# Optimization experiments

Hardware: AMD Instinct MI355X
Metric: run time of the kernel (lower is better)

The kernel has to match this reference:

```python
import jax, jax.numpy as jnp
import numpy as np

SEG = 8  # conv1d groups


def _grouped_mix(y, W2, b2, seg):
    # y: [b, C_in, L]; W2: [C_out, C_in//seg]; grouped 1x1 conv1d
    b_, cin, L = y.shape
    cout = W2.shape[0]
    yg = y.reshape(b_, seg, cin // seg, L)
    Wg = W2.reshape(seg, cout // seg, cin // seg)
    z = jnp.einsum('bgcl,goc->bgol', yg, Wg).reshape(b_, cout, L)
    return z + b2[None, :, None]


def _mix_h(x, W1, b1, W2, b2):
    # x: [b,h,w,d]
    b_, H, Wd, D = x.shape
    y = jnp.einsum('bhwd,ed->bhwe', x, W1) + b1            # 1x1 conv2d -> [b,h,w,e]
    y = jnp.transpose(y, (0, 3, 1, 2)).reshape(b_, -1, Wd)  # 'b d h w -> b (d h) w'
    z = _grouped_mix(y, W2, b2, SEG)                        # [b, h*h, w]
    attn = jax.nn.softmax(
        z.reshape(b_, H, H, Wd).transpose(0, 3, 1, 2), axis=-1)  # [b,w,h1,h2]
    xr = jnp.transpose(x, (0, 2, 1, 3))                     # [b,w,h,d]
    out = jnp.einsum('bwij,bwjd->bwid', attn, xr)
    return jnp.transpose(out, (0, 2, 1, 3))                 # [b,h,w,d]


def _mix_w(x, W1, b1, W2, b2):
    # x: [b,h,w,d]
    b_, H, Wd, D = x.shape
    y = jnp.einsum('bhwd,ed->bhwe', x, W1) + b1             # [b,h,w,e]
    y = jnp.transpose(y, (0, 3, 2, 1)).reshape(b_, -1, H)   # 'b d w h -> b (d w) h'
    z = _grouped_mix(y, W2, b2, SEG)                        # [b, w*w, h]
    attn = jax.nn.softmax(
        z.reshape(b_, Wd, Wd, H).transpose(0, 3, 1, 2), axis=-1)  # [b,h,w1,w2]
    return jnp.einsum('bhij,bhjd->bhid', attn, x)           # [b,h,w,d]


def setup_inputs() -> dict:
    key = jax.random.key(0)
    ks = jax.random.split(key, 16)
    B, H, W, D, E = 64, 32, 32, 384, 2
    s = 0.05
    return {
        'x':   jax.random.normal(ks[0], (B, H, W, D), jnp.float32),
        'Wc':  jax.random.normal(ks[1], (D, D), jnp.float32) * s,
        'bc':  jnp.zeros((D,), jnp.float32),
        'Wo':  jax.random.normal(ks[2], (D, D), jnp.float32) * s,
        'bo':  jnp.zeros((D,), jnp.float32),
        'W1h': jax.random.normal(ks[3], (E, D), jnp.float32) * s,
        'b1h': jnp.zeros((E,), jnp.float32),
        'W2h': jax.random.normal(ks[4], (H * H, E * H // SEG), jnp.float32) * s,
        'b2h': jnp.zeros((H * H,), jnp.float32),
        'W1w': jax.random.normal(ks[5], (E, D), jnp.float32) * s,
        'b1w': jnp.zeros((E,), jnp.float32),
        'W2w': jax.random.normal(ks[6], (W * W, E * W // SEG), jnp.float32) * s,
        'b2w': jnp.zeros((W * W,), jnp.float32),
    }


def reference(x, Wc, bc, Wo, bo, W1h, b1h, W2h, b2h, W1w, b1w, W2w, b2w):
    Y_c = jnp.einsum('bhwd,od->bhwo', x, Wc) + bc
    Y_h = _mix_h(x, W1h, b1h, W2h, b2h)
    Y_w = _mix_w(x, W1w, b1w, W2w, b2w)
    Y = Y_h + Y_w + Y_c
    return jnp.einsum('bhwd,od->bhwo', Y, Wo) + bo
```

## Files before the change

### kernel.cpp

```cpp
#include <hip/hip_runtime.h>
#include <hip/hip_bf16.h>
#include <cstdint>
#include <cstddef>

typedef __bf16 bf16;
typedef __attribute__((ext_vector_type(8))) __bf16 bf16x8;
typedef __attribute__((ext_vector_type(4))) float floatx4;

#define NPIX 65536

__device__ inline void async_copy16(void* lds, const void* g) {
    __builtin_amdgcn_global_load_lds(
        (const __attribute__((address_space(1))) void*)g,
        (__attribute__((address_space(3))) void*)lds, 16, 0, 0);
}

__global__ void k_prep_w(const float* __restrict__ Wc, const float* __restrict__ bc,
                         const float* __restrict__ Wo, const float* __restrict__ bo,
                         bf16* __restrict__ Wfull, float* __restrict__ bco) {
    int blk = blockIdx.x;
    int t = threadIdx.x;
    if (blk < 384) {
        int o = blk;
        float acc = 0.f;
        for (int d = 0; d < 384; ++d)
            acc += Wo[o * 384 + d] * Wc[d * 384 + t];
        Wfull[(size_t)o * 768 + t]       = (bf16)Wo[o * 384 + t];
        Wfull[(size_t)o * 768 + 384 + t] = (bf16)acc;
    } else {
        int o = t;
        float acc = bo[o];
        for (int d = 0; d < 384; ++d)
            acc += Wo[o * 384 + d] * bc[d];
        bco[o] = acc;
    }
}

__global__ void k_proj(const float* __restrict__ xf, bf16* __restrict__ xb,
                       const float* __restrict__ W1h, const float* __restrict__ b1h,
                       const float* __restrict__ W1w, const float* __restrict__ b1w,
                       float* __restrict__ yh, float* __restrict__ yw) {
    int t  = threadIdx.x;
    int lg = t & 7;
    int pg = t >> 3;
    int p  = blockIdx.x * 32 + pg;
    int b = p >> 10, h = (p >> 5) & 31, w = p & 31;
    const float4* xp4 = (const float4*)(xf + (size_t)p * 384);
    float a0 = 0.f, a1 = 0.f, a2 = 0.f, a3 = 0.f;
#pragma unroll
    for (int j = 0; j < 6; ++j) {
        int c = j * 8 + lg;
        float4 xa = xp4[c * 2], xcv = xp4[c * 2 + 1];
        bf16x8 v;
        v[0] = (bf16)xa.x; v[1] = (bf16)xa.y; v[2] = (bf16)xa.z; v[3] = (bf16)xa.w;
        v[4] = (bf16)xcv.x; v[5] = (bf16)xcv.y; v[6] = (bf16)xcv.z; v[7] = (bf16)xcv.w;
        *(bf16x8*)(xb + (size_t)p * 384 + c * 8) = v;
        const float4* h0 = (const float4*)(W1h + c * 8);
        const float4* h1 = (const float4*)(W1h + 384 + c * 8);
        const float4* w0 = (const float4*)(W1w + c * 8);
        const float4* w1 = (const float4*)(W1w + 384 + c * 8);
        float4 h0a = h0[0], h0b = h0[1], h1a = h1[0], h1b = h1[1];
        float4 w0a = w0[0], w0b = w0[1], w1a = w1[0], w1b = w1[1];
        a0 += xa.x*h0a.x + xa.y*h0a.y + xa.z*h0a.z + xa.w*h0a.w
            + xcv.x*h0b.x + xcv.y*h0b.y + xcv.z*h0b.z + xcv.w*h0b.w;
        a1 += xa.x*h1a.x + xa.y*h1a.y + xa.z*h1a.z + xa.w*h1a.w
            + xcv.x*h1b.x + xcv.y*h1b.y + xcv.z*h1b.z + xcv.w*h1b.w;
        a2 += xa.x*w0a.x + xa.y*w0a.y + xa.z*w0a.z + xa.w*w0a.w
            + xcv.x*w0b.x + xcv.y*w0b.y + xcv.z*w0b.z + xcv.w*w0b.w;
        a3 += xa.x*w1a.x + xa.y*w1a.y + xa.z*w1a.z + xa.w*w1a.w
            + xcv.x*w1b.x + xcv.y*w1b.y + xcv.z*w1b.z + xcv.w*w1b.w;
    }
#pragma unroll
    for (int m = 1; m < 8; m <<= 1) {
        a0 += __shfl_xor(a0, m, 64);
        a1 += __shfl_xor(a1, m, 64);
        a2 += __shfl_xor(a2, m, 64);
        a3 += __shfl_xor(a3, m, 64);
    }
    if (lg == 0) {
        yh[((b * 2 + 0) * 32 + h) * 32 + w] = a0 + b1h[0];
        yh[((b * 2 + 1) * 32 + h) * 32 + w] = a1 + b1h[1];
        yw[((b * 2 + 0) * 32 + w) * 32 + h] = a2 + b1w[0];
        yw[((b * 2 + 1) * 32 + w) * 32 + h] = a3 + b1w[1];
    }
}

__global__ void k_attn(const float* __restrict__ yproj,
                       const float* __restrict__ W2, const float* __restrict__ b2,
                       bf16* __restrict__ attn) {
    int blk = blockIdx.x;
    int bi = blk >> 5, r1 = blk & 31;
    int g = r1 >> 2;
    int cb = g * 8;
    int e = cb >> 5, rb = cb & 31;
    int lane = threadIdx.x;
    int l = lane & 31, half = lane >> 5;
    float yv[8];
    const float* ybase = yproj + (((bi * 2 + e) * 32 + rb) * 32 + l);
#pragma unroll
    for (int c = 0; c < 8; ++c) yv[c] = ybase[c * 32];
    float z[16];
#pragma unroll
    for (int jj = 0; jj < 16; ++jj) {
        int r2 = half * 16 + jj;
        int row = r1 * 32 + r2;
        const float4* wp = (const float4*)(W2 + (size_t)row * 8);
        float4 wa = wp[0], wb = wp[1];
        z[jj] = b2[row]
              + yv[0]*wa.x + yv[1]*wa.y + yv[2]*wa.z + yv[3]*wa.w
              + yv[4]*wb.x + yv[5]*wb.y + yv[6]*wb.z + yv[7]*wb.w;
    }
    float m = -1e30f;
#pragma unroll
    for (int jj = 0; jj < 16; ++jj) m = fmaxf(m, z[jj]);
    m = fmaxf(m, __shfl_xor(m, 32, 64));
    float s = 0.f;
#pragma unroll
    for (int jj = 0; jj < 16; ++jj) { z[jj] = __expf(z[jj] - m); s += z[jj]; }
    s += __shfl_xor(s, 32, 64);
    float inv = 1.f / s;
    bf16x8 o0, o1;
#pragma unroll
    for (int jj = 0; jj < 8; ++jj) o0[jj] = (bf16)(z[jj] * inv);
#pragma unroll
    for (int jj = 0; jj < 8; ++jj) o1[jj] = (bf16)(z[8 + jj] * inv);
    bf16x8* dst = (bf16x8*)(attn + ((((size_t)bi * 32 + l) * 32 + r1) * 32 + half * 16));
    dst[0] = o0;
    dst[1] = o1;
}

__global__ __launch_bounds__(256) void k_mix(const bf16* __restrict__ x,
                                             const bf16* __restrict__ attn_h,
                                             const bf16* __restrict__ attn_w,
                                             bf16* __restrict__ T) {
    __shared__ bf16 Xs[1024 * 16];
    __shared__ bf16 Ts[1024 * 16];
    int n = blockIdx.x;
    int a = n >> 5, r = n & 31;
    int q = a * 8 + (r & 7);
    int bi = q / 6, cq = q % 6;
    int c = cq * 4 + (r >> 3);
    int dbase = c * 16;
    int tid = threadIdx.x;
    int wv = tid >> 6, lane = tid & 63;
    int n16 = lane & 15, quad = lane >> 4;

    const char* gbase = (const char*)(x + (size_t)bi * 1024 * 384 + dbase);
#pragma unroll
    for (int it = 0; it < 8; ++it) {
        int p0 = wv * 256 + it * 32;
        const char* g = gbase + (size_t)(p0 + (lane >> 1)) * 768 + (lane & 1) * 16;
        char* l = (char*)Xs + p0 * 32 + lane * 16;
        async_copy16(l, g);
    }
    __syncthreads();

#pragma unroll
    for (int wl = 0; wl < 8; ++wl) {
        int w = wv * 8 + wl;
        const bf16* ab = attn_h + ((size_t)(bi * 32 + w) * 32) * 32;
        bf16x8 af0 = *(const bf16x8*)(ab + n16 * 32 + quad * 8);
        bf16x8 af1 = *(const bf16x8*)(ab + (16 + n16) * 32 + quad * 8);
        bf16x8 bfrag;
#pragma unroll
        for (int i = 0; i < 8; ++i) {
            int j = quad * 8 + i;
            bfrag[i] = Xs[(j * 32 + w) * 16 + n16];
        }
        floatx4 c0 = {0.f, 0.f, 0.f, 0.f}, c1 = {0.f, 0.f, 0.f, 0.f};
        c0 = __builtin_amdgcn_mfma_f32_16x16x32_bf16(af0, bfrag, c0, 0, 0, 0);
        c1 = __builtin_amdgcn_mfma_f32_16x16x32_bf16(af1, bfrag, c1, 0, 0, 0);
#pragma unroll
        for (int rr = 0; rr < 4; ++rr) {
            int h0 = quad * 4 + rr;
            Ts[(h0 * 32 + w) * 16 + n16]        = (bf16)c0[rr];
            Ts[((16 + h0) * 32 + w) * 16 + n16] = (bf16)c1[rr];
        }
    }
    __syncthreads();

#pragma unroll
    for (int hl = 0; hl < 8; ++hl) {
        int h = wv * 8 + hl;
        const bf16* ab = attn_w + ((size_t)(bi * 32 + h) * 32) * 32;
        bf16x8 af0 = *(const bf16x8*)(ab + n16 * 32 + quad * 8);
        bf16x8 af1 = *(const bf16x8*)(ab + (16 + n16) * 32 + quad * 8);
        bf16x8 bfrag;
#pragma unroll
        for (int i = 0; i < 8; ++i) {
            int j = quad * 8 + i;
            bfrag[i] = Xs[(h * 32 + j) * 16 + n16];
        }
        floatx4 c0 = {0.f, 0.f, 0.f, 0.f}, c1 = {0.f, 0.f, 0.f, 0.f};
        c0 = __builtin_amdgcn_mfma_f32_16x16x32_bf16(af0, bfrag, c0, 0, 0, 0);
        c1 = __builtin_amdgcn_mfma_f32_16x16x32_bf16(af1, bfrag, c1, 0, 0, 0);
        bf16* Tr = T + ((size_t)(bi * 32 + h) * 32) * 384 + dbase;
#pragma unroll
        for (int rr = 0; rr < 4; ++rr) {
            int w0 = quad * 4 + rr;
            Tr[(size_t)w0 * 384 + n16] =
                (bf16)(c0[rr] + (float)Ts[(h * 32 + w0) * 16 + n16]);
            Tr[(size_t)(16 + w0) * 384 + n16] =
                (bf16)(c1[rr] + (float)Ts[(h * 32 + 16 + w0) * 16 + n16]);
        }
    }
}

#define LDP 72
__global__ __launch_bounds__(256) void k_gemm(const bf16* __restrict__ T, const bf16* __restrict__ x,
                                              const bf16* __restrict__ Wfull, const float* __restrict__ bco,
                                              float* __restrict__ out) {
    __shared__ bf16 As[128 * LDP];
    __shared__ bf16 Bs[128 * LDP];
    int bx = blockIdx.x;
    int gid = (bx & 7) * 192 + (bx >> 3);
    int nt = gid % 3, pt = gid / 3;
    int obase = nt * 128;
    int pbase = pt * 128;
    int tid = threadIdx.x;
    int wv = tid >> 6, lane = tid & 63;
    int wm = wv & 1, wn = wv >> 1;
    int n16 = lane & 15, quad = lane >> 4;
    int lrow = tid >> 3;
    int lchunk = tid & 7;
    floatx4 zero = {0.f, 0.f, 0.f, 0.f};
    floatx4 acc[4][4];
#pragma unroll
    for (int i = 0; i < 4; ++i)
#pragma unroll
        for (int j = 0; j < 4; ++j) acc[i][j] = zero;

    for (int kt = 0; kt < 12; ++kt) {
        const bf16* Asrc = (kt < 6) ? (T + (size_t)pbase * 384 + kt * 64)
                                    : (x + (size_t)pbase * 384 + (kt - 6) * 64);
        const bf16* Bsrc = Wfull + (size_t)obase * 768 + kt * 64;
        bf16x8 av[4], bv[4];
#pragma unroll
        for (int s = 0; s < 4; ++s)
            av[s] = *(const bf16x8*)(Asrc + (size_t)(s * 32 + lrow) * 384 + lchunk * 8);
#pragma unroll
        for (int s = 0; s < 4; ++s)
            bv[s] = *(const bf16x8*)(Bsrc + (size_t)(s * 32 + lrow) * 768 + lchunk * 8);
        __syncthreads();
#pragma unroll
        for (int s = 0; s < 4; ++s)
            *(bf16x8*)(As + (s * 32 + lrow) * LDP + lchunk * 8) = av[s];
#pragma unroll
        for (int s = 0; s < 4; ++s)
            *(bf16x8*)(Bs + (s * 32 + lrow) * LDP + lchunk * 8) = bv[s];
        __syncthreads();
#pragma unroll
        for (int ks = 0; ks < 2; ++ks) {
            bf16x8 a[4], b[4];
#pragma unroll
            for (int i = 0; i < 4; ++i)
                a[i] = *(const bf16x8*)(As + (wm * 64 + i * 16 + n16) * LDP + ks * 32 + quad * 8);
#pragma unroll
            for (int i = 0; i < 4; ++i)
                b[i] = *(const bf16x8*)(Bs + (wn * 64 + i * 16 + n16) * LDP + ks * 32 + quad * 8);
#pragma unroll
            for (int i = 0; i < 4; ++i)
#pragma unroll
                for (int j = 0; j < 4; ++j)
                    acc[i][j] = __builtin_amdgcn_mfma_f32_16x16x32_bf16(a[i], b[j], acc[i][j], 0, 0, 0);
        }
    }
#pragma unroll
    for (int j = 0; j < 4; ++j) {
        int o = obase + wn * 64 + j * 16 + n16;
        float bcv = bco[o];
#pragma unroll
        for (int i = 0; i < 4; ++i) {
            int prow = pbase + wm * 64 + i * 16 + quad * 4;
#pragma unroll
            for (int r = 0; r < 4; ++r)
                out[(size_t)(prow + r) * 384 + o] = acc[i][j][r] + bcv;
        }
    }
}

extern "C" void kernel_launch(void* const* d_in, const int* in_sizes, int n_in,
                              void* d_out, int out_size, void* d_ws, size_t ws_size,
                              hipStream_t stream) {
    const float* x   = (const float*)d_in[0];
    const float* Wc  = (const float*)d_in[1];
    const float* bc  = (const float*)d_in[2];
    const float* Wo  = (const float*)d_in[3];
    const float* bo  = (const float*)d_in[4];
    const float* W1h = (const float*)d_in[5];
    const float* b1h = (const float*)d_in[6];
    const float* W2h = (const float*)d_in[7];
    const float* b2h = (const float*)d_in[8];
    const float* W1w = (const float*)d_in[9];
    const float* b1w = (const float*)d_in[10];
    const float* W2w = (const float*)d_in[11];
    const float* b2w = (const float*)d_in[12];
    float* out = (float*)d_out;

    char* ws = (char*)d_ws;
    size_t off = 0;
    auto alloc = [&](size_t bytes) {
        void* p = ws + off;
        off = (off + bytes + 255) & ~(size_t)255;
        return p;
    };
    bf16*  xb     = (bf16*)alloc((size_t)NPIX * 384 * 2);
    float* yh     = (float*)alloc((size_t)131072 * 4);
    float* yw     = (float*)alloc((size_t)131072 * 4);
    bf16*  attn_h = (bf16*)alloc((size_t)2097152 * 2);
    bf16*  attn_w = (bf16*)alloc((size_t)2097152 * 2);
    bf16*  T      = (bf16*)alloc((size_t)NPIX * 384 * 2);
    bf16*  Wfull  = (bf16*)alloc((size_t)384 * 768 * 2);
    float* bco    = (float*)alloc((size_t)384 * 4);

    hipLaunchKernelGGL(k_prep_w, dim3(385), dim3(384), 0, stream, Wc, bc, Wo, bo, Wfull, bco);
    hipLaunchKernelGGL(k_proj, dim3(2048), dim3(256), 0, stream, x, xb, W1h, b1h, W1w, b1w, yh, yw);
    hipLaunchKernelGGL(k_attn, dim3(2048), dim3(64), 0, stream, yh, W2h, b2h, attn_h);
    hipLaunchKernelGGL(k_attn, dim3(2048), dim3(64), 0, stream, yw, W2w, b2w, attn_w);
    hipLaunchKernelGGL(k_mix, dim3(1536), dim3(256), 0, stream, xb, attn_h, attn_w, T);
    hipLaunchKernelGGL(k_gemm, dim3(1536), dim3(256), 0, stream, T, xb, Wfull, bco, out);
}
```

Baseline: 324.4 us.

## Use channel-blocked bf16 layout and double-buffered async LDS loads in GEMM

```diff
diff --git a/kernel.cpp b/kernel.cpp
--- a/kernel.cpp
+++ b/kernel.cpp
@@ -54,7 +54,7 @@
         bf16x8 v;
         v[0] = (bf16)xa.x; v[1] = (bf16)xa.y; v[2] = (bf16)xa.z; v[3] = (bf16)xa.w;
         v[4] = (bf16)xcv.x; v[5] = (bf16)xcv.y; v[6] = (bf16)xcv.z; v[7] = (bf16)xcv.w;
-        *(bf16x8*)(xb + (size_t)p * 384 + c * 8) = v;
+        *(bf16x8*)(xb + ((size_t)(c >> 1) * NPIX + p) * 16 + (c & 1) * 8) = v;
         const float4* h0 = (const float4*)(W1h + c * 8);
         const float4* h1 = (const float4*)(W1h + 384 + c * 8);
         const float4* w0 = (const float4*)(W1w + c * 8);
@@ -136,23 +136,18 @@
     __shared__ bf16 Xs[1024 * 16];
     __shared__ bf16 Ts[1024 * 16];
     int n = blockIdx.x;
-    int a = n >> 5, r = n & 31;
-    int q = a * 8 + (r & 7);
-    int bi = q / 6, cq = q % 6;
-    int c = cq * 4 + (r >> 3);
-    int dbase = c * 16;
+    int idx = n >> 3;
+    int bi = (n & 7) * 8 + idx / 24;
+    int c  = idx % 24;
     int tid = threadIdx.x;
     int wv = tid >> 6, lane = tid & 63;
     int n16 = lane & 15, quad = lane >> 4;
 
-    const char* gbase = (const char*)(x + (size_t)bi * 1024 * 384 + dbase);
-#pragma unroll
-    for (int it = 0; it < 8; ++it) {
-        int p0 = wv * 256 + it * 32;
-        const char* g = gbase + (size_t)(p0 + (lane >> 1)) * 768 + (lane & 1) * 16;
-        char* l = (char*)Xs + p0 * 32 + lane * 16;
-        async_copy16(l, g);
-    }
+    const bf16* src = x + ((size_t)c * NPIX + bi * 1024) * 16;
+#pragma unroll
+    for (int it = 0; it < 8; ++it)
+        async_copy16((char*)Xs + (it * 256 + tid) * 16,
+                     (const char*)src + (size_t)(it * 256 + tid) * 16);
     __syncthreads();
 
 #pragma unroll
@@ -194,24 +189,29 @@
         floatx4 c0 = {0.f, 0.f, 0.f, 0.f}, c1 = {0.f, 0.f, 0.f, 0.f};
         c0 = __builtin_amdgcn_mfma_f32_16x16x32_bf16(af0, bfrag, c0, 0, 0, 0);
         c1 = __builtin_amdgcn_mfma_f32_16x16x32_bf16(af1, bfrag, c1, 0, 0, 0);
-        bf16* Tr = T + ((size_t)(bi * 32 + h) * 32) * 384 + dbase;
 #pragma unroll
         for (int rr = 0; rr < 4; ++rr) {
             int w0 = quad * 4 + rr;
-            Tr[(size_t)w0 * 384 + n16] =
+            Xs[(h * 32 + w0) * 16 + n16] =
                 (bf16)(c0[rr] + (float)Ts[(h * 32 + w0) * 16 + n16]);
-            Tr[(size_t)(16 + w0) * 384 + n16] =
+            Xs[(h * 32 + 16 + w0) * 16 + n16] =
                 (bf16)(c1[rr] + (float)Ts[(h * 32 + 16 + w0) * 16 + n16]);
         }
     }
-}
-
-#define LDP 72
+    __syncthreads();
+
+    bf16* dst = T + ((size_t)c * NPIX + bi * 1024) * 16;
+#pragma unroll
+    for (int it = 0; it < 8; ++it)
+        *(bf16x8*)(dst + (size_t)(it * 256 + tid) * 8) =
+            *(const bf16x8*)(Xs + (it * 256 + tid) * 8);
+}
+
 __global__ __launch_bounds__(256) void k_gemm(const bf16* __restrict__ T, const bf16* __restrict__ x,
                                               const bf16* __restrict__ Wfull, const float* __restrict__ bco,
                                               float* __restrict__ out) {
-    __shared__ bf16 As[128 * LDP];
-    __shared__ bf16 Bs[128 * LDP];
+    __shared__ bf16 As[2][128 * 64];
+    __shared__ bf16 Bs[2][128 * 64];
     int bx = blockIdx.x;
     int gid = (bx & 7) * 192 + (bx >> 3);
     int nt = gid % 3, pt = gid / 3;
@@ -221,8 +221,7 @@
     int wv = tid >> 6, lane = tid & 63;
     int wm = wv & 1, wn = wv >> 1;
     int n16 = lane & 15, quad = lane >> 4;
-    int lrow = tid >> 3;
-    int lchunk = tid & 7;
+    int srow = lane >> 3, sch = lane & 7;
     floatx4 zero = {0.f, 0.f, 0.f, 0.f};
     floatx4 acc[4][4];
 #pragma unroll
@@ -230,40 +229,43 @@
 #pragma unroll
         for (int j = 0; j < 4; ++j) acc[i][j] = zero;
 
+    const bf16* Bg0 = Wfull + (size_t)obase * 768;
+
+    auto stage = [&](int buf, int kt) {
+        const bf16* Ag = (kt < 6) ? T : x;
+        size_t arow = ((size_t)(((kt < 6) ? kt : kt - 6) * 4 + (sch >> 1))) * NPIX + pbase;
+#pragma unroll
+        for (int it = 0; it < 4; ++it) {
+            int r0 = wv * 32 + it * 8;
+            async_copy16((void*)(As[buf] + r0 * 64 + lane * 8),
+                         (const void*)(Ag + (arow + r0 + srow) * 16 + (sch & 1) * 8));
+            async_copy16((void*)(Bs[buf] + r0 * 64 + lane * 8),
+                         (const void*)(Bg0 + (size_t)(r0 + srow) * 768 + kt * 64 + sch * 8));
+        }
+    };
+
+    stage(0, 0);
+    __syncthreads();
+    int buf = 0;
     for (int kt = 0; kt < 12; ++kt) {
-        const bf16* Asrc = (kt < 6) ? (T + (size_t)pbase * 384 + kt * 64)
-                                    : (x + (size_t)pbase * 384 + (kt - 6) * 64);
-        const bf16* Bsrc = Wfull + (size_t)obase * 768 + kt * 64;
-        bf16x8 av[4], bv[4];
-#pragma unroll
-        for (int s = 0; s < 4; ++s)
-            av[s] = *(const bf16x8*)(Asrc + (size_t)(s * 32 + lrow) * 384 + lchunk * 8);
-#pragma unroll
-        for (int s = 0; s < 4; ++s)
-            bv[s] = *(const bf16x8*)(Bsrc + (size_t)(s * 32 + lrow) * 768 + lchunk * 8);
-        __syncthreads();
-#pragma unroll
-        for (int s = 0; s < 4; ++s)
-            *(bf16x8*)(As + (s * 32 + lrow) * LDP + lchunk * 8) = av[s];
-#pragma unroll
-        for (int s = 0; s < 4; ++s)
-            *(bf16x8*)(Bs + (s * 32 + lrow) * LDP + lchunk * 8) = bv[s];
-        __syncthreads();
+        if (kt < 11) stage(buf ^ 1, kt + 1);
 #pragma unroll
         for (int ks = 0; ks < 2; ++ks) {
             bf16x8 a[4], b[4];
 #pragma unroll
             for (int i = 0; i < 4; ++i)
-                a[i] = *(const bf16x8*)(As + (wm * 64 + i * 16 + n16) * LDP + ks * 32 + quad * 8);
-#pragma unroll
-            for (int i = 0; i < 4; ++i)
-                b[i] = *(const bf16x8*)(Bs + (wn * 64 + i * 16 + n16) * LDP + ks * 32 + quad * 8);
+                a[i] = *(const bf16x8*)(As[buf] + (wm * 64 + i * 16 + n16) * 64 + ks * 32 + quad * 8);
+#pragma unroll
+            for (int j = 0; j < 4; ++j)
+                b[j] = *(const bf16x8*)(Bs[buf] + (wn * 64 + j * 16 + n16) * 64 + ks * 32 + quad * 8);
 #pragma unroll
             for (int i = 0; i < 4; ++i)
 #pragma unroll
                 for (int j = 0; j < 4; ++j)
                     acc[i][j] = __builtin_amdgcn_mfma_f32_16x16x32_bf16(a[i], b[j], acc[i][j], 0, 0, 0);
         }
+        __syncthreads();
+        buf ^= 1;
     }
 #pragma unroll
     for (int j = 0; j < 4; ++j) {
```

After: 341.6 us. 5.3% more time.
